# Kernel tuning notes

Hardware: AMD Instinct MI355X
Metric: run time of the kernel (lower is better)

## Reference

```python
import jax, jax.numpy as jnp
import numpy as np
from jax import lax

# Config mirrors TemporalLePEAttention(dim=256, resolution=(56,56), idx=0, split_size=4, num_heads=8, temporal=True)
B, T, H, W, C = 2, 2, 56, 56, 256
NH = 8
HD = C // NH
SS = 4                      # split_size
H_sp, W_sp = H, SS          # idx == 0 -> strip windows of full height
nWh, nWw = H // H_sp, W // W_sp   # 1, 14
SCALE = HD ** -0.5
KH, KW = W_sp, H_sp         # unfold kernel = focal_window = [W_sp, H_sp] = (4, 56)
PH, PW = 0, H_sp // 2       # idx == 0 padding = [0, H_sp//2]
NW = B * nWh * nWw          # number of windows
TQ = T * H_sp * W_sp        # query tokens per window


def setup_inputs() -> dict:
    key = jax.random.key(0)
    k1, k2 = jax.random.split(key, 2)
    qkv = jax.random.normal(k1, (3, B, T, H, W, C), jnp.float32)
    # depthwise 3x3 LePE conv (nn.Conv2d(dim, dim, 3, padding=1, groups=dim))
    get_v_w = jax.random.normal(k2, (C, 1, 3, 3), jnp.float32) * 0.1
    get_v_b = jnp.zeros((C,), jnp.float32)
    # pool linear initialized as in the module: weight = SS/(H_sp*W_sp), bias = 0
    pool_w = jnp.full((SS, H_sp * W_sp), SS / (H_sp * W_sp), jnp.float32)
    pool_b = jnp.zeros((SS,), jnp.float32)
    return {"qkv": qkv, "get_v_w": get_v_w, "get_v_b": get_v_b,
            "pool_w": pool_w, "pool_b": pool_b}


def _windows_thw(x):
    # im2ddca_temporal: (B,T,H,W,C) -> (B*nWh*nWw, NH, T*H_sp*W_sp, HD)
    x = x.reshape(B, T, nWh, H_sp, nWw, W_sp, C).transpose(0, 2, 4, 1, 3, 5, 6)
    x = x.reshape(NW, TQ, NH, HD).transpose(0, 2, 1, 3)
    return x


def _lepe_temporal(v, w, b):
    # get_lepe_temporal: window v, depthwise 3x3 conv, return (v_win, lepe) as (NW, NH, TQ, HD)
    xw = v.reshape(B, T, nWh, H_sp, nWw, W_sp, C).transpose(0, 2, 4, 1, 6, 3, 5)
    xw = xw.reshape(-1, C, H_sp, W_sp)  # (B*nWh*nWw*T, C, H_sp, W_sp)
    lepe = lax.conv_general_dilated(xw, w, (1, 1), 'SAME', feature_group_count=C,
                                    dimension_numbers=('NCHW', 'OIHW', 'NCHW'))
    lepe = lepe + b[None, :, None, None]

    def fmt(t):
        t = t.reshape(NW, T, NH, HD, H_sp * W_sp).transpose(0, 2, 1, 4, 3)
        return t.reshape(NW, NH, TQ, HD)
    return fmt(xw), fmt(lepe)


def _pool_unfold(t, pool_w, pool_b):
    # focal pooling: per-window linear over H_sp*W_sp -> SS, then unfold over pooled map
    tw = t.reshape(B, T, nWh, H_sp, nWw, W_sp, C).transpose(0, 2, 4, 1, 6, 3, 5)
    tw = tw.reshape(B, nWh, nWw, T, C, H_sp * W_sp)
    p = jnp.einsum('bhwtcn,sn->bhwtcs', tw, pool_w) + pool_b  # (B,nWh,nWw,T,C,SS)
    # flatten(-2) + permute + reshape -> pooled map (B*T, C, SS*nWh, nWw)  (idx == 0)
    pm = p.transpose(0, 3, 4, 5, 1, 2).reshape(B * T, C, SS * nWh, nWw)
    # nn.Unfold(kernel=(KH,KW), padding=(PH,PW), stride=1); here out_h == 1
    pmp = jnp.pad(pm, ((0, 0), (0, 0), (PH, PH), (PW, PW)))
    ow = pmp.shape[3] - KW + 1  # = nWw + 1
    patches = jnp.stack([pmp[:, :, :, i:i + KW] for i in range(ow)], axis=1)  # (BT, ow, C, KH, KW)
    u = patches.reshape(B, T, ow, C, KH, KW).transpose(0, 2, 1, 4, 5, 3)      # (B, ow, T, KH, KW, C)
    u = u.reshape(B * ow, T * KH * KW, NH, HD).transpose(0, 2, 1, 3)          # (B*ow, NH, Tkk, HD)
    # idx == 0: view (B, nWh, -1, ...) and drop the last unfold location -> one per window
    u = u.reshape(B, nWh, ow // nWh, NH, T * KH * KW, HD)[:, :, :-1]
    return u.reshape(NW, NH, T * KH * KW, HD)


def reference(qkv, get_v_w, get_v_b, pool_w, pool_b):
    q_in, k_in, v_in = qkv[0], qkv[1], qkv[2]
    q = _windows_thw(q_in) * SCALE                      # (NW, NH, TQ, HD)
    k = _windows_thw(k_in)
    v, lepe = _lepe_temporal(v_in, get_v_w, get_v_b)
    kp = _pool_unfold(k_in, pool_w, pool_b)             # (NW, NH, TQ, HD)
    vp = _pool_unfold(v_in, pool_w, pool_b)
    k = jnp.concatenate([k, kp], axis=2)                # (NW, NH, 2*TQ, HD)
    v = jnp.concatenate([v, vp], axis=2)
    attn = jax.nn.softmax(jnp.einsum('wnqd,wnkd->wnqk', q, k), axis=-1)
    x = jnp.einsum('wnqk,wnkd->wnqd', attn, v) + lepe   # (NW, NH, TQ, HD)
    x = x.transpose(0, 2, 1, 3).reshape(NW, TQ, C)
    # windows2img_temporal -> (B, T, H, W, C)
    x = x.reshape(B, nWh, nWw, T, H_sp, W_sp, C).transpose(0, 3, 1, 4, 2, 5, 6)
    return x.reshape(B, T, H, W, C)
```

## Files before the change

### kernel.cpp

```cpp
#include <hip/hip_runtime.h>
#include <hip/hip_bf16.h>

#define B_   2
#define T_   2
#define H_   56
#define W_   56
#define C_   256
#define NH_  8
#define HD_  32
#define NWW_ 14
#define TQ_  448
#define SEQ_ 576
#define REAL_ 560
#define VIRT_ 320.0f
#define MEXP_ 16.0f
#define PMSTR_ 57344

typedef __bf16 bf16;
typedef __bf16 bf16x8 __attribute__((ext_vector_type(8)));
typedef __bf16 bf16x4 __attribute__((ext_vector_type(4)));
typedef float  f32x4  __attribute__((ext_vector_type(4)));
typedef short  s16x4  __attribute__((ext_vector_type(4)));
typedef unsigned int  uint;
typedef uint   uint4v __attribute__((ext_vector_type(4)));
typedef uint   uint2v __attribute__((ext_vector_type(2)));
typedef unsigned short u16;

#if defined(__has_builtin)
#  if __has_builtin(__builtin_amdgcn_mfma_f32_16x16x16bf16_1k)
#    define USE_MFMA16 1
#  endif
#endif
#ifndef USE_MFMA16
#  define USE_MFMA16 0
#endif

__device__ __forceinline__ uint pack2(float a, float b) {
    u16 ha = __builtin_bit_cast(u16, (bf16)a);
    u16 hb = __builtin_bit_cast(u16, (bf16)b);
    return (uint)ha | ((uint)hb << 16);
}

__global__ void pre_kernel(const float* __restrict__ k_in, const float* __restrict__ v_in,
                           const float* __restrict__ pool_w, const float* __restrict__ pool_b,
                           const float* __restrict__ gw, const float* __restrict__ gb,
                           float* __restrict__ pmk_part, float* __restrict__ pmv_part,
                           bf16* __restrict__ lepe) {
    __shared__ float pws[4][56];
    const int bid = blockIdx.x;
    const int c   = threadIdx.x;

    if (bid < 224) {
        const int quarter = bid & 3;
        const int bj = bid >> 2;
        const int j  = bj % NWW_;
        const int t  = (bj / NWW_) % T_;
        const int b  = bj / (NWW_ * T_);
        const int n0 = quarter * 56;

        if (c < 224) pws[c / 56][c % 56] = pool_w[(c / 56) * 224 + n0 + (c % 56)];
        __syncthreads();

        float ak[4], av[4];
        #pragma unroll
        for (int s = 0; s < 4; ++s) {
            ak[s] = (quarter == 0) ? pool_b[s] : 0.f;
            av[s] = 0.f;
        }
        for (int i = 0; i < 56; ++i) {
            const int n = n0 + i;
            const int h = n >> 2, wi = n & 3;
            const size_t off = ((size_t)(((b * T_ + t) * H_ + h) * W_ + (j * 4 + wi))) * C_ + c;
            const float kv = k_in[off];
            const float vv = v_in[off];
            #pragma unroll
            for (int s = 0; s < 4; ++s) {
                ak[s] += kv * pws[s][i];
                av[s] += vv * pws[s][i];
            }
        }
        #pragma unroll
        for (int s = 0; s < 4; ++s) {
            const size_t o = (size_t)quarter * PMSTR_ +
                             ((size_t)(((b * T_ + t) * 4 + s) * NWW_ + j)) * C_ + c;
            pmk_part[o] = ak[s];
            pmv_part[o] = av[s];
        }
    } else {
        const int r  = bid - 224;
        const int sp = r % 7;
        const int h  = (r / 7) % H_;
        const int bt = r / (7 * H_);

        float wv9[9];
        #pragma unroll
        for (int k = 0; k < 9; ++k) wv9[k] = gw[c * 9 + k];
        const float bias = gb[c];

        #pragma unroll
        for (int s2 = 0; s2 < 2; ++s2) {
            const int strip = sp * 2 + s2;
            float tile[3][4];
            #pragma unroll
            for (int dy = 0; dy < 3; ++dy) {
                const int hh = h - 1 + dy;
                const bool ok = (hh >= 0 && hh < H_);
                #pragma unroll
                for (int x = 0; x < 4; ++x) {
                    tile[dy][x] = ok
                        ? v_in[((size_t)(bt * H_ + hh) * W_ + (strip * 4 + x)) * C_ + c]
                        : 0.f;
                }
            }
            #pragma unroll
            for (int wi = 0; wi < 4; ++wi) {
                float acc = bias;
                #pragma unroll
                for (int dy = 0; dy < 3; ++dy) {
                    #pragma unroll
                    for (int dx = -1; dx <= 1; ++dx) {
                        const int xx = wi + dx;
                        if (xx >= 0 && xx < 4)
                            acc += wv9[dy * 3 + dx + 1] * tile[dy][xx];
                    }
                }
                lepe[((size_t)(bt * H_ + h) * W_ + (strip * 4 + wi)) * C_ + c] = (bf16)acc;
            }
        }
    }
}

__launch_bounds__(768, 1)
__global__ void attn_kernel(const float* __restrict__ q_in, const float* __restrict__ k_in,
                            const float* __restrict__ v_in, const float* __restrict__ pm_k,
                            const float* __restrict__ pm_v, const bf16* __restrict__ lepe,
                            float* __restrict__ out) {
    __shared__ __align__(16) u16 smem[66304];
    u16* Ks = smem;
    u16* Vt = smem + 23040;

    const int tid  = threadIdx.x;
    const int nh   = blockIdx.x & 7;
    const int nwi  = blockIdx.x >> 3;
    const int b    = nwi / NWW_;
    const int ww   = nwi % NWW_;
    const int cbase = nh * 32;

    for (int idx = tid; idx < SEQ_ * 4; idx += 768) {
        const int tok = idx >> 2, slot = idx & 3;
        uint4v dk = {0, 0, 0, 0}, dv = {0, 0, 0, 0};
        if (tok < TQ_) {
            const int t = tok / 224, r = tok % 224;
            const int h = r >> 2, wi = r & 3;
            const size_t off =
                ((size_t)(((b * T_ + t) * H_ + h) * W_ + (ww * 4 + wi))) * C_ + cbase + slot * 8;
            const f32x4 k0 = *(const f32x4*)(k_in + off);
            const f32x4 k1 = *(const f32x4*)(k_in + off + 4);
            const f32x4 v0 = *(const f32x4*)(v_in + off);
            const f32x4 v1 = *(const f32x4*)(v_in + off + 4);
            dk = uint4v{pack2(k0[0], k0[1]), pack2(k0[2], k0[3]),
                        pack2(k1[0], k1[1]), pack2(k1[2], k1[3])};
            dv = uint4v{pack2(v0[0], v0[1]), pack2(v0[2], v0[3]),
                        pack2(v1[0], v1[1]), pack2(v1[2], v1[3])};
        } else if (tok < REAL_) {
            const int i = tok - TQ_;
            const int t = i / 56, r = i % 56;
            const int kh = r / 14, jj = r % 14;
            const size_t off =
                ((size_t)(((b * T_ + t) * 4 + kh) * NWW_ + jj)) * C_ + cbase + slot * 8;
            f32x4 k0 = {0,0,0,0}, k1 = {0,0,0,0}, v0 = {0,0,0,0}, v1 = {0,0,0,0};
            #pragma unroll
            for (int pq = 0; pq < 4; ++pq) {
                const float* pk = pm_k + (size_t)pq * PMSTR_ + off;
                const float* pv = pm_v + (size_t)pq * PMSTR_ + off;
                k0 += *(const f32x4*)pk;  k1 += *(const f32x4*)(pk + 4);
                v0 += *(const f32x4*)pv;  v1 += *(const f32x4*)(pv + 4);
            }
            dk = uint4v{pack2(k0[0], k0[1]), pack2(k0[2], k0[3]),
                        pack2(k1[0], k1[1]), pack2(k1[2], k1[3])};
            dv = uint4v{pack2(v0[0], v0[1]), pack2(v0[2], v0[3]),
                        pack2(v1[0], v1[1]), pack2(v1[2], v1[3])};
        }
        *(uint4v*)(Ks + tok * 40 + slot * 8) = dk;
        u16 es[8];
        #pragma unroll
        for (int e = 0; e < 8; ++e) es[e] = (u16)((dv[e >> 1] >> ((e & 1) * 16)) & 0xffff);
        #pragma unroll
        for (int e = 0; e < 8; ++e) Vt[(slot * 8 + e) * 584 + tok] = es[e];
    }
    __syncthreads();

    const int lane = tid & 63;
    const int wv   = tid >> 6;
    const int qg   = wv & 3;
    const int seg  = wv >> 2;
    const int l15  = lane & 15;
    const int g    = lane >> 4;
    const float QS = 0.17677669529663687f * 1.4426950408889634f;

    bf16x8 qf[7];
    #pragma unroll
    for (int qt = 0; qt < 7; ++qt) {
        const int qrow = qg * 112 + qt * 16 + l15;
        const int t = qrow / 224, r = qrow % 224;
        const int h = r >> 2, wi = r & 3;
        const size_t off =
            ((size_t)(((b * T_ + t) * H_ + h) * W_ + (ww * 4 + wi))) * C_ + cbase + g * 8;
        const f32x4 a0 = *(const f32x4*)(q_in + off);
        const f32x4 a1 = *(const f32x4*)(q_in + off + 4);
        const uint4v qp = {pack2(a0[0] * QS, a0[1] * QS), pack2(a0[2] * QS, a0[3] * QS),
                           pack2(a1[0] * QS, a1[1] * QS), pack2(a1[2] * QS, a1[3] * QS)};
        qf[qt] = __builtin_bit_cast(bf16x8, qp);
    }

    f32x4 o[7][2];
    float ssum[7];
    const f32x4 zf = {0.f, 0.f, 0.f, 0.f};
    #pragma unroll
    for (int qt = 0; qt < 7; ++qt) {
        o[qt][0] = zf; o[qt][1] = zf; ssum[qt] = 0.f;
    }

    const int kc0 = seg * 6;
    for (int kc = kc0; kc < kc0 + 6; ++kc) {
        const int kt0 = kc * 32;
        const bf16x8 ka = *(const bf16x8*)(Ks + (kt0 + l15) * 40 + g * 8);
        const bf16x8 kb = *(const bf16x8*)(Ks + (kt0 + 16 + l15) * 40 + g * 8);
#if USE_MFMA16
        const s16x4 va00 = __builtin_bit_cast(s16x4, *(const uint2v*)(Vt + l15 * 584 + kt0 + g * 4));
        const s16x4 va01 = __builtin_bit_cast(s16x4, *(const uint2v*)(Vt + l15 * 584 + kt0 + 16 + g * 4));
        const s16x4 va10 = __builtin_bit_cast(s16x4, *(const uint2v*)(Vt + (16 + l15) * 584 + kt0 + g * 4));
        const s16x4 va11 = __builtin_bit_cast(s16x4, *(const uint2v*)(Vt + (16 + l15) * 584 + kt0 + 16 + g * 4));
#else
        const bf16x8 va = *(const bf16x8*)(Vt + l15 * 584 + kt0 + g * 8);
        const bf16x8 vb = *(const bf16x8*)(Vt + (16 + l15) * 584 + kt0 + g * 8);
#endif

        #pragma unroll
        for (int qt = 0; qt < 7; ++qt) {
            const f32x4 s0 = __builtin_amdgcn_mfma_f32_16x16x32_bf16(ka, qf[qt], zf, 0, 0, 0);
            const f32x4 s1 = __builtin_amdgcn_mfma_f32_16x16x32_bf16(kb, qf[qt], zf, 0, 0, 0);

            const float p0 = __builtin_amdgcn_exp2f(s0[0] - MEXP_);
            const float p1 = __builtin_amdgcn_exp2f(s0[1] - MEXP_);
            const float p2 = __builtin_amdgcn_exp2f(s0[2] - MEXP_);
            const float p3 = __builtin_amdgcn_exp2f(s0[3] - MEXP_);
            const float p4 = __builtin_amdgcn_exp2f(s1[0] - MEXP_);
            const float p5 = __builtin_amdgcn_exp2f(s1[1] - MEXP_);
            const float p6 = __builtin_amdgcn_exp2f(s1[2] - MEXP_);
            const float p7 = __builtin_amdgcn_exp2f(s1[3] - MEXP_);

            ssum[qt] += ((p0 + p1) + (p2 + p3)) + ((p4 + p5) + (p6 + p7));

            const uint w0 = pack2(p0, p1), w1 = pack2(p2, p3);
            const uint w2 = pack2(p4, p5), w3 = pack2(p6, p7);
#if USE_MFMA16
            const s16x4 pb0 = __builtin_bit_cast(s16x4, uint2v{w0, w1});
            const s16x4 pb1 = __builtin_bit_cast(s16x4, uint2v{w2, w3});
            o[qt][0] = __builtin_amdgcn_mfma_f32_16x16x16bf16_1k(va00, pb0, o[qt][0], 0, 0, 0);
            o[qt][0] = __builtin_amdgcn_mfma_f32_16x16x16bf16_1k(va01, pb1, o[qt][0], 0, 0, 0);
            o[qt][1] = __builtin_amdgcn_mfma_f32_16x16x16bf16_1k(va10, pb0, o[qt][1], 0, 0, 0);
            o[qt][1] = __builtin_amdgcn_mfma_f32_16x16x16bf16_1k(va11, pb1, o[qt][1], 0, 0, 0);
#else
            const int baseln = l15 + ((g & 1) << 5);
            const uint sA = (g & 2) ? w2 : w0;
            const uint sB = (g & 2) ? w3 : w1;
            const uint o0 = (uint)__shfl((int)sA, baseln);
            const uint o1 = (uint)__shfl((int)sB, baseln);
            const uint o2 = (uint)__shfl((int)sA, baseln + 16);
            const uint o3 = (uint)__shfl((int)sB, baseln + 16);
            const bf16x8 pf = __builtin_bit_cast(bf16x8, uint4v{o0, o1, o2, o3});
            o[qt][0] = __builtin_amdgcn_mfma_f32_16x16x32_bf16(pf, va, o[qt][0], 0, 0, 0);
            o[qt][1] = __builtin_amdgcn_mfma_f32_16x16x32_bf16(pf, vb, o[qt][1], 0, 0, 0);
#endif
        }
    }

    float sred[7];
    #pragma unroll
    for (int qt = 0; qt < 7; ++qt) {
        float s = ssum[qt];
        s += __shfl_xor(s, 16);
        s += __shfl_xor(s, 32);
        sred[qt] = s;
    }

    __syncthreads();

    float* opart = (float*)smem;
    float* ssp   = opart + 2 * 16128;

    if (seg > 0) {
        const int so = (seg - 1) * 16128;
#if USE_MFMA16
        #pragma unroll
        for (int qt = 0; qt < 7; ++qt) {
            const int q = qg * 112 + qt * 16 + l15;
            *(f32x4*)(opart + so + q * 36 + g * 4)      = o[qt][0];
            *(f32x4*)(opart + so + q * 36 + 16 + g * 4) = o[qt][1];
        }
        if (g == 0) {
            #pragma unroll
            for (int qt = 0; qt < 7; ++qt)
                ssp[(seg - 1) * 448 + qg * 112 + qt * 16 + l15] = sred[qt];
        }
#else
        #pragma unroll
        for (int qt = 0; qt < 7; ++qt) {
            #pragma unroll
            for (int r = 0; r < 4; ++r) {
                const int q = qg * 112 + qt * 16 + g * 4 + r;
                opart[so + q * 36 + l15]      = o[qt][0][r];
                opart[so + q * 36 + l15 + 16] = o[qt][1][r];
            }
        }
        if (g == 0) {
            #pragma unroll
            for (int qt = 0; qt < 7; ++qt)
                ssp[(seg - 1) * 448 + qg * 112 + qt * 16 + l15] = sred[qt];
        }
#endif
    }
    __syncthreads();

    if (seg == 0) {
        #pragma unroll
        for (int qt = 0; qt < 7; ++qt) {
            const int q = qg * 112 + qt * 16 + l15;
            const float den = sred[qt] + ssp[q] + ssp[448 + q]
                            + VIRT_ * 0.0000152587890625f;
            const float osc = 1.0f / den;

#if USE_MFMA16
            const int t = q / 224, rr = q % 224;
            const int h = rr >> 2, wi = rr & 3;
            const size_t off =
                ((size_t)(((b * T_ + t) * H_ + h) * W_ + (ww * 4 + wi))) * C_ + cbase;
            #pragma unroll
            for (int h2 = 0; h2 < 2; ++h2) {
                const int co = h2 * 16 + g * 4;
                const f32x4 pa = *(const f32x4*)(opart + q * 36 + co);
                const f32x4 pb = *(const f32x4*)(opart + 16128 + q * 36 + co);
                const bf16x4 lp = *(const bf16x4*)(lepe + off + co);
                f32x4 val;
                #pragma unroll
                for (int r = 0; r < 4; ++r)
                    val[r] = (o[qt][h2][r] + pa[r] + pb[r]) * osc + (float)lp[r];
                *(f32x4*)(out + off + co) = val;
            }
#else
            #pragma unroll
            for (int r = 0; r < 4; ++r) {
                const float oscr = __shfl(osc, g * 4 + r);
                const int qrow = qg * 112 + qt * 16 + g * 4 + r;
                const int t = qrow / 224, rr = qrow % 224;
                const int h = rr >> 2, wi = rr & 3;
                const size_t off =
                    ((size_t)(((b * T_ + t) * H_ + h) * W_ + (ww * 4 + wi))) * C_ + cbase + l15;
                out[off] = (o[qt][0][r] + opart[qrow * 36 + l15] +
                            opart[16128 + qrow * 36 + l15]) * oscr + (float)lepe[off];
                out[off + 16] = (o[qt][1][r] + opart[qrow * 36 + l15 + 16] +
                                 opart[16128 + qrow * 36 + l15 + 16]) * oscr + (float)lepe[off + 16];
            }
#endif
        }
    }
}

extern "C" void kernel_launch(void* const* d_in, const int* in_sizes, int n_in,
                              void* d_out, int out_size, void* d_ws, size_t ws_size,
                              hipStream_t stream) {
    const float* qkv = (const float*)d_in[0];
    const float* gw  = (const float*)d_in[1];
    const float* gb  = (const float*)d_in[2];
    const float* pw  = (const float*)d_in[3];
    const float* pb  = (const float*)d_in[4];

    const size_t plane = (size_t)B_ * T_ * H_ * W_ * C_;
    const float* q_in = qkv;
    const float* k_in = qkv + plane;
    const float* v_in = qkv + 2 * plane;

    float* pmk_part = (float*)d_ws;
    float* pmv_part = pmk_part + 4 * PMSTR_;
    bf16*  lepe     = (bf16*)(pmv_part + 4 * PMSTR_);
    float* outp     = (float*)d_out;

    hipLaunchKernelGGL(pre_kernel, dim3(224 + 1568), dim3(256), 0, stream,
                       k_in, v_in, pw, pb, gw, gb, pmk_part, pmv_part, lepe);
    hipLaunchKernelGGL(attn_kernel, dim3(28 * 8), dim3(768), 0, stream,
                       q_in, k_in, v_in, pmk_part, pmv_part, lepe, outp);
}
```

Baseline: 47.27 us.

## Split attention work by query tiles across 14 waves, drop key-split reduction

Reworks the attention kernel so each of 14 waves owns two 16-row query tiles and walks the full key sequence, rather than 12 waves splitting keys into 3 segments over 7 query tiles each. This removes the shared-memory partial-output reduction, the extra barriers and the large LDS scratch buffer, and cuts per-wave register pressure so occupancy can rise. In exchange each wave re-reads all K/V fragments from LDS with less reuse per load, and the block grows to 896 threads.

```diff
diff --git a/kernel.cpp b/kernel.cpp
--- a/kernel.cpp
+++ b/kernel.cpp
@@ -130,14 +130,13 @@
     }
 }
 
-__launch_bounds__(768, 1)
+__launch_bounds__(896, 4)
 __global__ void attn_kernel(const float* __restrict__ q_in, const float* __restrict__ k_in,
                             const float* __restrict__ v_in, const float* __restrict__ pm_k,
                             const float* __restrict__ pm_v, const bf16* __restrict__ lepe,
                             float* __restrict__ out) {
-    __shared__ __align__(16) u16 smem[66304];
-    u16* Ks = smem;
-    u16* Vt = smem + 23040;
+    __shared__ __align__(16) u16 Ks[SEQ_ * 40];
+    __shared__ __align__(16) u16 Vt[32 * 584];
 
     const int tid  = threadIdx.x;
     const int nh   = blockIdx.x & 7;
@@ -146,7 +145,7 @@
     const int ww   = nwi % NWW_;
     const int cbase = nh * 32;
 
-    for (int idx = tid; idx < SEQ_ * 4; idx += 768) {
+    for (int idx = tid; idx < SEQ_ * 4; idx += 896) {
         const int tok = idx >> 2, slot = idx & 3;
         uint4v dk = {0, 0, 0, 0}, dv = {0, 0, 0, 0};
         if (tok < TQ_) {
@@ -192,16 +191,14 @@
 
     const int lane = tid & 63;
     const int wv   = tid >> 6;
-    const int qg   = wv & 3;
-    const int seg  = wv >> 2;
     const int l15  = lane & 15;
     const int g    = lane >> 4;
     const float QS = 0.17677669529663687f * 1.4426950408889634f;
 
-    bf16x8 qf[7];
+    bf16x8 qf[2];
     #pragma unroll
-    for (int qt = 0; qt < 7; ++qt) {
-        const int qrow = qg * 112 + qt * 16 + l15;
+    for (int ti = 0; ti < 2; ++ti) {
+        const int qrow = (wv + ti * 14) * 16 + l15;
         const int t = qrow / 224, r = qrow % 224;
         const int h = r >> 2, wi = r & 3;
         const size_t off =
@@ -210,19 +207,18 @@
         const f32x4 a1 = *(const f32x4*)(q_in + off + 4);
         const uint4v qp = {pack2(a0[0] * QS, a0[1] * QS), pack2(a0[2] * QS, a0[3] * QS),
                            pack2(a1[0] * QS, a1[1] * QS), pack2(a1[2] * QS, a1[3] * QS)};
-        qf[qt] = __builtin_bit_cast(bf16x8, qp);
-    }
-
-    f32x4 o[7][2];
-    float ssum[7];
+        qf[ti] = __builtin_bit_cast(bf16x8, qp);
+    }
+
+    f32x4 o[2][2];
+    float ssum[2];
     const f32x4 zf = {0.f, 0.f, 0.f, 0.f};
     #pragma unroll
-    for (int qt = 0; qt < 7; ++qt) {
-        o[qt][0] = zf; o[qt][1] = zf; ssum[qt] = 0.f;
-    }
-
-    const int kc0 = seg * 6;
-    for (int kc = kc0; kc < kc0 + 6; ++kc) {
+    for (int ti = 0; ti < 2; ++ti) {
+        o[ti][0] = zf; o[ti][1] = zf; ssum[ti] = 0.f;
+    }
+
+    for (int kc = 0; kc < SEQ_ / 32; ++kc) {
         const int kt0 = kc * 32;
         const bf16x8 ka = *(const bf16x8*)(Ks + (kt0 + l15) * 40 + g * 8);
         const bf16x8 kb = *(const bf16x8*)(Ks + (kt0 + 16 + l15) * 40 + g * 8);
@@ -237,9 +233,9 @@
 #endif
 
         #pragma unroll
-        for (int qt = 0; qt < 7; ++qt) {
-            const f32x4 s0 = __builtin_amdgcn_mfma_f32_16x16x32_bf16(ka, qf[qt], zf, 0, 0, 0);
-            const f32x4 s1 = __builtin_amdgcn_mfma_f32_16x16x32_bf16(kb, qf[qt], zf, 0, 0, 0);
+        for (int ti = 0; ti < 2; ++ti) {
+            const f32x4 s0 = __builtin_amdgcn_mfma_f32_16x16x32_bf16(ka, qf[ti], zf, 0, 0, 0);
+            const f32x4 s1 = __builtin_amdgcn_mfma_f32_16x16x32_bf16(kb, qf[ti], zf, 0, 0, 0);
 
             const float p0 = __builtin_amdgcn_exp2f(s0[0] - MEXP_);
             const float p1 = __builtin_amdgcn_exp2f(s0[1] - MEXP_);
@@ -250,17 +246,17 @@
             const float p6 = __builtin_amdgcn_exp2f(s1[2] - MEXP_);
             const float p7 = __builtin_amdgcn_exp2f(s1[3] - MEXP_);
 
-            ssum[qt] += ((p0 + p1) + (p2 + p3)) + ((p4 + p5) + (p6 + p7));
+            ssum[ti] += ((p0 + p1) + (p2 + p3)) + ((p4 + p5) + (p6 + p7));
 
             const uint w0 = pack2(p0, p1), w1 = pack2(p2, p3);
             const uint w2 = pack2(p4, p5), w3 = pack2(p6, p7);
 #if USE_MFMA16
             const s16x4 pb0 = __builtin_bit_cast(s16x4, uint2v{w0, w1});
             const s16x4 pb1 = __builtin_bit_cast(s16x4, uint2v{w2, w3});
-            o[qt][0] = __builtin_amdgcn_mfma_f32_16x16x16bf16_1k(va00, pb0, o[qt][0], 0, 0, 0);
-            o[qt][0] = __builtin_amdgcn_mfma_f32_16x16x16bf16_1k(va01, pb1, o[qt][0], 0, 0, 0);
-            o[qt][1] = __builtin_amdgcn_mfma_f32_16x16x16bf16_1k(va10, pb0, o[qt][1], 0, 0, 0);
-            o[qt][1] = __builtin_amdgcn_mfma_f32_16x16x16bf16_1k(va11, pb1, o[qt][1], 0, 0, 0);
+            o[ti][0] = __builtin_amdgcn_mfma_f32_16x16x16bf16_1k(va00, pb0, o[ti][0], 0, 0, 0);
+            o[ti][0] = __builtin_amdgcn_mfma_f32_16x16x16bf16_1k(va01, pb1, o[ti][0], 0, 0, 0);
+            o[ti][1] = __builtin_amdgcn_mfma_f32_16x16x16bf16_1k(va10, pb0, o[ti][1], 0, 0, 0);
+            o[ti][1] = __builtin_amdgcn_mfma_f32_16x16x16bf16_1k(va11, pb1, o[ti][1], 0, 0, 0);
 #else
             const int baseln = l15 + ((g & 1) << 5);
             const uint sA = (g & 2) ? w2 : w0;
@@ -270,100 +266,48 @@
             const uint o2 = (uint)__shfl((int)sA, baseln + 16);
             const uint o3 = (uint)__shfl((int)sB, baseln + 16);
             const bf16x8 pf = __builtin_bit_cast(bf16x8, uint4v{o0, o1, o2, o3});
-            o[qt][0] = __builtin_amdgcn_mfma_f32_16x16x32_bf16(pf, va, o[qt][0], 0, 0, 0);
-            o[qt][1] = __builtin_amdgcn_mfma_f32_16x16x32_bf16(pf, vb, o[qt][1], 0, 0, 0);
-#endif
-        }
-    }
-
-    float sred[7];
+            o[ti][0] = __builtin_amdgcn_mfma_f32_16x16x32_bf16(pf, va, o[ti][0], 0, 0, 0);
+            o[ti][1] = __builtin_amdgcn_mfma_f32_16x16x32_bf16(pf, vb, o[ti][1], 0, 0, 0);
+#endif
+        }
+    }
+
     #pragma unroll
-    for (int qt = 0; qt < 7; ++qt) {
-        float s = ssum[qt];
-        s += __shfl_xor(s, 16);
-        s += __shfl_xor(s, 32);
-        sred[qt] = s;
-    }
-
-    __syncthreads();
-
-    float* opart = (float*)smem;
-    float* ssp   = opart + 2 * 16128;
-
-    if (seg > 0) {
-        const int so = (seg - 1) * 16128;
+    for (int ti = 0; ti < 2; ++ti) {
+        float den = ssum[ti];
+        den += __shfl_xor(den, 16);
+        den += __shfl_xor(den, 32);
+        den += VIRT_ * 0.0000152587890625f;
+        const float osc = 1.0f / den;
+
 #if USE_MFMA16
-        #pragma unroll
-        for (int qt = 0; qt < 7; ++qt) {
-            const int q = qg * 112 + qt * 16 + l15;
-            *(f32x4*)(opart + so + q * 36 + g * 4)      = o[qt][0];
-            *(f32x4*)(opart + so + q * 36 + 16 + g * 4) = o[qt][1];
-        }
-        if (g == 0) {
-            #pragma unroll
-            for (int qt = 0; qt < 7; ++qt)
-                ssp[(seg - 1) * 448 + qg * 112 + qt * 16 + l15] = sred[qt];
+        const int qrow = (wv + ti * 14) * 16 + l15;
+        const int t = qrow / 224, rr = qrow % 224;
+        const int h = rr >> 2, wi = rr & 3;
+        const size_t off =
+            ((size_t)(((b * T_ + t) * H_ + h) * W_ + (ww * 4 + wi))) * C_ + cbase;
+        #pragma unroll
+        for (int h2 = 0; h2 < 2; ++h2) {
+            const int co = h2 * 16 + g * 4;
+            const bf16x4 lp = *(const bf16x4*)(lepe + off + co);
+            f32x4 val;
+            #pragma unroll
+            for (int r = 0; r < 4; ++r) val[r] = o[ti][h2][r] * osc + (float)lp[r];
+            *(f32x4*)(out + off + co) = val;
         }
 #else
         #pragma unroll
-        for (int qt = 0; qt < 7; ++qt) {
-            #pragma unroll
-            for (int r = 0; r < 4; ++r) {
-                const int q = qg * 112 + qt * 16 + g * 4 + r;
-                opart[so + q * 36 + l15]      = o[qt][0][r];
-                opart[so + q * 36 + l15 + 16] = o[qt][1][r];
-            }
-        }
-        if (g == 0) {
-            #pragma unroll
-            for (int qt = 0; qt < 7; ++qt)
-                ssp[(seg - 1) * 448 + qg * 112 + qt * 16 + l15] = sred[qt];
-        }
-#endif
-    }
-    __syncthreads();
-
-    if (seg == 0) {
-        #pragma unroll
-        for (int qt = 0; qt < 7; ++qt) {
-            const int q = qg * 112 + qt * 16 + l15;
-            const float den = sred[qt] + ssp[q] + ssp[448 + q]
-                            + VIRT_ * 0.0000152587890625f;
-            const float osc = 1.0f / den;
-
-#if USE_MFMA16
-            const int t = q / 224, rr = q % 224;
+        for (int r = 0; r < 4; ++r) {
+            const float oscr = __shfl(osc, g * 4 + r);
+            const int qrow = (wv + ti * 14) * 16 + g * 4 + r;
+            const int t = qrow / 224, rr = qrow % 224;
             const int h = rr >> 2, wi = rr & 3;
             const size_t off =
-                ((size_t)(((b * T_ + t) * H_ + h) * W_ + (ww * 4 + wi))) * C_ + cbase;
-            #pragma unroll
-            for (int h2 = 0; h2 < 2; ++h2) {
-                const int co = h2 * 16 + g * 4;
-                const f32x4 pa = *(const f32x4*)(opart + q * 36 + co);
-                const f32x4 pb = *(const f32x4*)(opart + 16128 + q * 36 + co);
-                const bf16x4 lp = *(const bf16x4*)(lepe + off + co);
-                f32x4 val;
-                #pragma unroll
-                for (int r = 0; r < 4; ++r)
-                    val[r] = (o[qt][h2][r] + pa[r] + pb[r]) * osc + (float)lp[r];
-                *(f32x4*)(out + off + co) = val;
-            }
-#else
-            #pragma unroll
-            for (int r = 0; r < 4; ++r) {
-                const float oscr = __shfl(osc, g * 4 + r);
-                const int qrow = qg * 112 + qt * 16 + g * 4 + r;
-                const int t = qrow / 224, rr = qrow % 224;
-                const int h = rr >> 2, wi = rr & 3;
-                const size_t off =
-                    ((size_t)(((b * T_ + t) * H_ + h) * W_ + (ww * 4 + wi))) * C_ + cbase + l15;
-                out[off] = (o[qt][0][r] + opart[qrow * 36 + l15] +
-                            opart[16128 + qrow * 36 + l15]) * oscr + (float)lepe[off];
-                out[off + 16] = (o[qt][1][r] + opart[qrow * 36 + l15 + 16] +
-                                 opart[16128 + qrow * 36 + l15 + 16]) * oscr + (float)lepe[off + 16];
-            }
-#endif
-        }
+                ((size_t)(((b * T_ + t) * H_ + h) * W_ + (ww * 4 + wi))) * C_ + cbase + l15;
+            out[off]      = o[ti][0][r] * oscr + (float)lepe[off];
+            out[off + 16] = o[ti][1][r] * oscr + (float)lepe[off + 16];
+        }
+#endif
     }
 }
 
@@ -388,6 +332,6 @@
 
     hipLaunchKernelGGL(pre_kernel, dim3(224 + 1568), dim3(256), 0, stream,
                        k_in, v_in, pw, pb, gw, gb, pmk_part, pmv_part, lepe);
-    hipLaunchKernelGGL(attn_kernel, dim3(28 * 8), dim3(768), 0, stream,
+    hipLaunchKernelGGL(attn_kernel, dim3(28 * 8), dim3(896), 0, stream,
                        q_in, k_in, v_in, pmk_part, pmv_part, lepe, outp);
 }
```

Result: faster. 44.51 us (-5.8%).
